# Performance work log

Hardware: AMD Instinct MI355X
Metric: run time of the kernel (lower is better)

The kernel has to match this reference:

```python
import jax, jax.numpy as jnp
import numpy as np
from jax.ops import segment_sum, segment_max

N = 50000
E = 800000
IN_C, HID_C, OUT_C, HEADS = 64, 128, 32, 4
BN_EPS = 1e-5
NEG_SLOPE = 0.2


def setup_inputs() -> dict:
    key = jax.random.key(0)
    ks = jax.random.split(key, 16)
    s = 0.1  # weight scale for numerical sanity
    inp = {
        'x': jax.random.normal(ks[0], (N, IN_C), jnp.float32),
        'edge_index': jax.random.randint(ks[1], (2, E), 0, N, jnp.int64),
        'sage1_wl': jax.random.normal(ks[2], (IN_C, HID_C), jnp.float32) * s,
        'sage1_bl': jnp.zeros((HID_C,), jnp.float32),
        'sage1_wr': jax.random.normal(ks[3], (IN_C, HID_C), jnp.float32) * s,
        'bn1_gamma': jnp.ones((HID_C,), jnp.float32),
        'bn1_beta': jnp.zeros((HID_C,), jnp.float32),
        'bn1_mean': jnp.zeros((HID_C,), jnp.float32),
        'bn1_var': jnp.ones((HID_C,), jnp.float32),
        'sage2_wl': jax.random.normal(ks[4], (HID_C, HID_C), jnp.float32) * s,
        'sage2_bl': jnp.zeros((HID_C,), jnp.float32),
        'sage2_wr': jax.random.normal(ks[5], (HID_C, HID_C), jnp.float32) * s,
        'bn2_gamma': jnp.ones((HID_C,), jnp.float32),
        'bn2_beta': jnp.zeros((HID_C,), jnp.float32),
        'bn2_mean': jnp.zeros((HID_C,), jnp.float32),
        'bn2_var': jnp.ones((HID_C,), jnp.float32),
        'gat_w': jax.random.normal(ks[6], (HID_C, HEADS * OUT_C), jnp.float32) * s,
        'gat_att_src': jax.random.normal(ks[7], (HEADS, OUT_C), jnp.float32) * s,
        'gat_att_dst': jax.random.normal(ks[8], (HEADS, OUT_C), jnp.float32) * s,
        'gat_bias': jnp.zeros((OUT_C,), jnp.float32),
        'cls_w1': jax.random.normal(ks[9], (OUT_C, 64), jnp.float32) * s,
        'cls_b1': jnp.zeros((64,), jnp.float32),
        'cls_w2': jax.random.normal(ks[10], (64, 1), jnp.float32) * s,
        'cls_b2': jnp.zeros((1,), jnp.float32),
    }
    return inp


def _sage_conv(x, src, dst, n, wl, bl, wr):
    # PyG SAGEConv (mean aggr): lin_l(mean_{j in N(i)} x_j) + lin_r(x_i)
    agg = segment_sum(x[src], dst, num_segments=n)           # [N, C]
    cnt = segment_sum(jnp.ones((src.shape[0], 1), x.dtype), dst, num_segments=n)
    mean = agg / jnp.maximum(cnt, 1.0)
    return mean @ wl + bl + x @ wr


def _bn_eval(x, gamma, beta, mean, var):
    return (x - mean) * jax.lax.rsqrt(var + BN_EPS) * gamma + beta


def _gat_conv(x, src, dst, n, w, att_src, att_dst, bias):
    # PyG GATConv, concat=False (head-average), add_self_loops=True
    loop = jnp.arange(n, dtype=src.dtype)
    s = jnp.concatenate([src, loop])
    d = jnp.concatenate([dst, loop])
    h = (x @ w).reshape(n, HEADS, OUT_C)                     # [N, H, C]
    a_src = jnp.einsum('nhc,hc->nh', h, att_src)             # [N, H]
    a_dst = jnp.einsum('nhc,hc->nh', h, att_dst)             # [N, H]
    e = jax.nn.leaky_relu(a_src[s] + a_dst[d], NEG_SLOPE)    # [Etot, H]
    m = segment_max(e, d, num_segments=n)                    # stable softmax per dst
    ex = jnp.exp(e - m[d])
    den = segment_sum(ex, d, num_segments=n)
    alpha = ex / den[d]                                      # [Etot, H]
    out = segment_sum(alpha[:, :, None] * h[s], d, num_segments=n)  # [N, H, C]
    return out.mean(axis=1) + bias                           # concat=False -> mean over heads


def reference(x, edge_index,
              sage1_wl, sage1_bl, sage1_wr,
              bn1_gamma, bn1_beta, bn1_mean, bn1_var,
              sage2_wl, sage2_bl, sage2_wr,
              bn2_gamma, bn2_beta, bn2_mean, bn2_var,
              gat_w, gat_att_src, gat_att_dst, gat_bias,
              cls_w1, cls_b1, cls_w2, cls_b2):
    n = x.shape[0]
    src, dst = edge_index[0], edge_index[1]
    # Layer 0: SAGE(64->128) + BN + ReLU (no residual: shapes differ); dropout = eval noop
    h = _sage_conv(x, src, dst, n, sage1_wl, sage1_bl, sage1_wr)
    h = jax.nn.relu(_bn_eval(h, bn1_gamma, bn1_beta, bn1_mean, bn1_var))
    # Layer 1: SAGE(128->128) + BN + residual + ReLU
    identity = h
    h2 = _sage_conv(h, src, dst, n, sage2_wl, sage2_bl, sage2_wr)
    h2 = _bn_eval(h2, bn2_gamma, bn2_beta, bn2_mean, bn2_var) + identity
    h2 = jax.nn.relu(h2)
    # Final layer: GAT head (128 -> 32, 4 heads averaged)
    embeddings = _gat_conv(h2, src, dst, n, gat_w, gat_att_src, gat_att_dst, gat_bias)
    # MLP classifier (dropout eval noop)
    logits = jax.nn.relu(embeddings @ cls_w1 + cls_b1) @ cls_w2 + cls_b2
    return embeddings, logits
```

## Files before the change

### kernel.cpp

```cpp
#include <hip/hip_runtime.h>

typedef unsigned int uint_t;
typedef unsigned short ush;
typedef short bf16x8 __attribute__((ext_vector_type(8)));
typedef float f32x4 __attribute__((ext_vector_type(4)));

constexpr int TPB = 256;
#define LOG2E 1.4426950408889634f

__device__ __forceinline__ float lrelu(float x){ return fmaxf(x, 0.f) + 0.2f*fminf(x, 0.f); }
__device__ __forceinline__ ush f2b(float f){
  uint_t u = __float_as_uint(f);
  return (ush)((u + 0x7fffu + ((u >> 16) & 1u)) >> 16);
}
__device__ __forceinline__ float b2f(ush s){ return __uint_as_float(((uint_t)s) << 16); }
__device__ __forceinline__ float eexp(float x){ return exp2f(x * LOG2E); }

__global__ void k_bnfold(const float* __restrict__ g1, const float* __restrict__ b1,
                         const float* __restrict__ m1, const float* __restrict__ v1,
                         const float* __restrict__ g2, const float* __restrict__ b2,
                         const float* __restrict__ m2, const float* __restrict__ v2,
                         float* __restrict__ out){
  int t = threadIdx.x;
  int o = t & 127;
  bool second = t >= 128;
  const float* g = second ? g2 : g1;  const float* b = second ? b2 : b1;
  const float* m = second ? m2 : m1;  const float* v = second ? v2 : v1;
  float sc = g[o] * rsqrtf(v[o] + 1e-5f);
  float sh = b[o] - m[o]*sc;
  int off = second ? 256 : 0;
  out[off + o] = sc;
  out[off + 128 + o] = sh;
}

__global__ void k_deg(const int* __restrict__ dst, int* __restrict__ degi, int E){
  int t = blockIdx.x*TPB + threadIdx.x;
  if (t < E) atomicAdd(&degi[dst[t]], 1);
}

__global__ __launch_bounds__(1024) void k_scan1(const int* __restrict__ deg,
                                                int* __restrict__ out,
                                                int* __restrict__ bsum, int n){
  __shared__ int ws[16];
  int tid = threadIdx.x;
  int gid = blockIdx.x*1024 + tid;
  int v = (gid < n) ? deg[gid] : 0;
  int lane = tid & 63, wid = tid >> 6;
  int s = v;
  for (int off = 1; off < 64; off <<= 1){
    int t2 = __shfl_up(s, off);
    if (lane >= off) s += t2;
  }
  if (lane == 63) ws[wid] = s;
  __syncthreads();
  if (wid == 0){
    int w = (lane < 16) ? ws[lane] : 0;
    for (int off = 1; off < 16; off <<= 1){
      int t2 = __shfl_up(w, off);
      if (lane >= off) w += t2;
    }
    if (lane < 16) ws[lane] = w;
  }
  __syncthreads();
  int base = wid > 0 ? ws[wid-1] : 0;
  int incl = base + s;
  if (gid < n) out[gid] = incl - v;
  if (tid == 1023) bsum[blockIdx.x] = incl;
}

__global__ void k_scan2(int* __restrict__ bsum, int nb){
  int lane = threadIdx.x;
  int carry = 0;
  for (int base = 0; base < nb; base += 64){
    int i = base + lane;
    int v = (i < nb) ? bsum[i] : 0;
    int s = v;
    for (int off = 1; off < 64; off <<= 1){
      int t2 = __shfl_up(s, off);
      if (lane >= off) s += t2;
    }
    if (i < nb) bsum[i] = carry + s - v;
    int tot = __shfl(s, 63);
    carry += tot;
  }
  if (lane == 0) bsum[nb] = carry;
}

__global__ void k_scan3(int* __restrict__ offs, const int* __restrict__ bsum, int n, int nb){
  int gid = blockIdx.x*TPB + threadIdx.x;
  if (gid < n) offs[gid] += bsum[gid >> 10];
  else if (gid == n) offs[n] = bsum[nb];
}

__global__ void k_fill(const int* __restrict__ src, const int* __restrict__ dst,
                       const int* __restrict__ offs, int* __restrict__ cur,
                       int* __restrict__ esrc, int E){
  int t = blockIdx.x*TPB + threadIdx.x;
  if (t >= E) return;
  int d = dst[t];
  int p = offs[d] + atomicAdd(&cur[d], 1);
  esrc[p] = src[t];
}

__global__ void k_tobf16(const float* __restrict__ in, ush* __restrict__ out, int n4){
  int t = blockIdx.x*TPB + threadIdx.x;
  if (t >= n4) return;
  float4 v = *(const float4*)(in + (size_t)t*4);
  ushort4 o;
  o.x = f2b(v.x); o.y = f2b(v.y); o.z = f2b(v.z); o.w = f2b(v.w);
  *(ushort4*)(out + (size_t)t*4) = o;
}

__global__ void k_wprep(const float* __restrict__ wr, const float* __restrict__ wl,
                        int C1, int K, ush* __restrict__ WT){
  int t = blockIdx.x*TPB + threadIdx.x;
  if (t >= 128*K) return;
  int n = t / K, k = t % K;
  float v = (k < C1) ? wr[(size_t)k*128 + n] : wl[(size_t)(k - C1)*128 + n];
  WT[t] = f2b(v);
}

template<int C>
__global__ __launch_bounds__(256) void k_gather_mean_b(
    const int* __restrict__ offs, const int* __restrict__ esrc,
    const uint_t* __restrict__ xb, uint_t* __restrict__ meanb, int n){
  constexpr int L = C/2;
  int tid = threadIdx.x;
  int nid = blockIdx.x*(256/L) + tid/L;
  int l = tid % L;
  if (nid >= n) return;
  int k0 = offs[nid], k1 = offs[nid+1];
  float s0 = 0.f, s1 = 0.f;
  int k = k0;
  for (; k + 4 <= k1; k += 4){
    int e0 = esrc[k], e1 = esrc[k+1], e2 = esrc[k+2], e3 = esrc[k+3];
    uint_t u0 = xb[(size_t)e0*L + l];
    uint_t u1 = xb[(size_t)e1*L + l];
    uint_t u2 = xb[(size_t)e2*L + l];
    uint_t u3 = xb[(size_t)e3*L + l];
    s0 += b2f((ush)(u0 & 0xffffu)) + b2f((ush)(u1 & 0xffffu))
        + b2f((ush)(u2 & 0xffffu)) + b2f((ush)(u3 & 0xffffu));
    s1 += b2f((ush)(u0 >> 16)) + b2f((ush)(u1 >> 16))
        + b2f((ush)(u2 >> 16)) + b2f((ush)(u3 >> 16));
  }
  for (; k < k1; ++k){
    uint_t u = xb[(size_t)esrc[k]*L + l];
    s0 += b2f((ush)(u & 0xffffu));
    s1 += b2f((ush)(u >> 16));
  }
  float inv = 1.f / (float)max(k1 - k0, 1);
  uint_t lo = f2b(s0*inv), hi = f2b(s1*inv);
  meanb[(size_t)nid*L + l] = lo | (hi << 16);
}

template<int K, bool BN, bool RES, bool RELU>
__global__ __launch_bounds__(256) void k_mm_mfma(
    const ush* __restrict__ A1, int C1,
    const ush* __restrict__ A2,
    const ush* __restrict__ WT,
    const float* __restrict__ bias,
    const float* __restrict__ bnp, int bnoff,
    const float* __restrict__ res,
    float* __restrict__ out, ush* __restrict__ outb, int n)
{
  constexpr int PAD = K + 8;
  __shared__ ush sA[32][PAD];
  int tid = threadIdx.x;
  int wave = tid >> 6, lane = tid & 63;
  int node0 = blockIdx.x * 32;
  int C2 = K - C1;

  for (int idx = tid; idx < 32*(K/8); idx += 256) {
    int r  = idx / (K/8);
    int kc = (idx % (K/8)) * 8;
    int g = node0 + r;
    uint4 v = make_uint4(0,0,0,0);
    if (g < n) {
      if (kc < C1) v = *(const uint4*)(A1 + (size_t)g*C1 + kc);
      else         v = *(const uint4*)(A2 + (size_t)g*C2 + (kc - C1));
    }
    *(uint4*)&sA[r][kc] = v;
  }
  __syncthreads();

  f32x4 acc[2][2] = {};
  int l15 = lane & 15, lk = (lane >> 4) * 8;
  const ush* wt0 = WT + (size_t)(wave*32 + l15) * K + lk;
  const ush* wt1 = wt0 + (size_t)16 * K;

  #pragma unroll
  for (int kk = 0; kk < K; kk += 32) {
    bf16x8 a0 = *(const bf16x8*)&sA[l15][kk + lk];
    bf16x8 a1 = *(const bf16x8*)&sA[16 + l15][kk + lk];
    bf16x8 b0 = *(const bf16x8*)(wt0 + kk);
    bf16x8 b1 = *(const bf16x8*)(wt1 + kk);
    acc[0][0] = __builtin_amdgcn_mfma_f32_16x16x32_bf16(a0, b0, acc[0][0], 0, 0, 0);
    acc[0][1] = __builtin_amdgcn_mfma_f32_16x16x32_bf16(a0, b1, acc[0][1], 0, 0, 0);
    acc[1][0] = __builtin_amdgcn_mfma_f32_16x16x32_bf16(a1, b0, acc[1][0], 0, 0, 0);
    acc[1][1] = __builtin_amdgcn_mfma_f32_16x16x32_bf16(a1, b1, acc[1][1], 0, 0, 0);
  }

  int r0 = (lane >> 4) * 4;
  #pragma unroll
  for (int mt = 0; mt < 2; ++mt) {
    #pragma unroll
    for (int nt = 0; nt < 2; ++nt) {
      int nn = wave*32 + nt*16 + l15;
      float bv = bias ? bias[nn] : 0.f;
      float sc = 1.f, sh = 0.f;
      if constexpr (BN) { sc = bnp[bnoff + nn]; sh = bnp[bnoff + 128 + nn]; }
      #pragma unroll
      for (int j = 0; j < 4; ++j) {
        int g = node0 + mt*16 + r0 + j;
        if (g < n) {
          float v = acc[mt][nt][j] + bv;
          if constexpr (BN)   v = v*sc + sh;
          if constexpr (RES)  v += res[(size_t)g*128 + nn];
          if constexpr (RELU) v = fmaxf(v, 0.f);
          if (out)  out[(size_t)g*128 + nn] = v;
          if (outb) outb[(size_t)g*128 + nn] = f2b(v);
        }
      }
    }
  }
}

__global__ void k_attn(const uint_t* __restrict__ hgb, const float* __restrict__ atts,
                       const float* __restrict__ attd, float* __restrict__ asrc,
                       float* __restrict__ adst, int n){
  int t = blockIdx.x*TPB + threadIdx.x;
  if (t >= n*4) return;
  int nid = t >> 2, h = t & 3;
  const uint_t* hp = hgb + (size_t)nid*64 + h*16;
  float as = 0.f, ad = 0.f;
  #pragma unroll
  for (int i = 0; i < 16; ++i) {
    uint_t u = hp[i];
    float v0 = b2f((ush)(u & 0xffffu));
    float v1 = b2f((ush)(u >> 16));
    as = fmaf(v0, atts[h*32 + 2*i],     as);
    as = fmaf(v1, atts[h*32 + 2*i + 1], as);
    ad = fmaf(v0, attd[h*32 + 2*i],     ad);
    ad = fmaf(v1, attd[h*32 + 2*i + 1], ad);
  }
  asrc[t] = as; adst[t] = ad;
}

__global__ __launch_bounds__(256) void k_gat(
    const int* __restrict__ offs, const int* __restrict__ esrc,
    const float* __restrict__ asrc, const float* __restrict__ adst,
    const uint_t* __restrict__ hgb, const float* __restrict__ gbias,
    const float* __restrict__ w1, const float* __restrict__ b1,
    const float* __restrict__ w2, const float* __restrict__ b2,
    float* __restrict__ out_emb, float* __restrict__ out_log, int n){
  __shared__ float semb[4][32];
  int tid = threadIdx.x;
  int wl = tid >> 6;
  int l = tid & 63;
  int nid = blockIdx.x*4 + wl;
  if (nid >= n) return;
  int h = l >> 4;
  int i4 = nid*4 + h;
  float ad = adst[i4];
  float e0 = eexp(lrelu(asrc[i4] + ad));
  uint_t u = hgb[(size_t)nid*64 + l];
  float accD  = e0;
  float accN0 = e0 * b2f((ush)(u & 0xffffu));
  float accN1 = e0 * b2f((ush)(u >> 16));
  int k0 = offs[nid], k1 = offs[nid+1];
  int k = k0;
  for (; k + 4 <= k1; k += 4){
    int s0 = esrc[k], s1 = esrc[k+1], s2 = esrc[k+2], s3 = esrc[k+3];
    float a0 = asrc[s0*4 + h], a1 = asrc[s1*4 + h];
    float a2 = asrc[s2*4 + h], a3 = asrc[s3*4 + h];
    uint_t v0 = hgb[(size_t)s0*64 + l];
    uint_t v1 = hgb[(size_t)s1*64 + l];
    uint_t v2 = hgb[(size_t)s2*64 + l];
    uint_t v3 = hgb[(size_t)s3*64 + l];
    float e0_ = eexp(lrelu(a0 + ad));
    float e1_ = eexp(lrelu(a1 + ad));
    float e2_ = eexp(lrelu(a2 + ad));
    float e3_ = eexp(lrelu(a3 + ad));
    accD += (e0_ + e1_) + (e2_ + e3_);
    accN0 = fmaf(e0_, b2f((ush)(v0 & 0xffffu)), accN0);
    accN0 = fmaf(e1_, b2f((ush)(v1 & 0xffffu)), accN0);
    accN0 = fmaf(e2_, b2f((ush)(v2 & 0xffffu)), accN0);
    accN0 = fmaf(e3_, b2f((ush)(v3 & 0xffffu)), accN0);
    accN1 = fmaf(e0_, b2f((ush)(v0 >> 16)), accN1);
    accN1 = fmaf(e1_, b2f((ush)(v1 >> 16)), accN1);
    accN1 = fmaf(e2_, b2f((ush)(v2 >> 16)), accN1);
    accN1 = fmaf(e3_, b2f((ush)(v3 >> 16)), accN1);
  }
  for (; k < k1; ++k){
    int s = esrc[k];
    float e = eexp(lrelu(asrc[s*4 + h] + ad));
    uint_t v = hgb[(size_t)s*64 + l];
    accD += e;
    accN0 = fmaf(e, b2f((ush)(v & 0xffffu)), accN0);
    accN1 = fmaf(e, b2f((ush)(v >> 16)),     accN1);
  }
  float inv = 1.f / accD;
  float v0 = accN0 * inv, v1 = accN1 * inv;
  v0 += __shfl_xor(v0, 16); v0 += __shfl_xor(v0, 32);
  v1 += __shfl_xor(v1, 16); v1 += __shfl_xor(v1, 32);
  if (l < 16){
    int c = l*2;
    float2 o;
    o.x = 0.25f*v0 + gbias[c];
    o.y = 0.25f*v1 + gbias[c+1];
    *(float2*)(out_emb + (size_t)nid*32 + c) = o;
    semb[wl][c] = o.x;
    semb[wl][c+1] = o.y;
  }
  float a = b1[l];
  #pragma unroll
  for (int c = 0; c < 32; ++c) a = fmaf(semb[wl][c], w1[c*64 + l], a);
  float t = fmaxf(a, 0.f) * w2[l];
  t += __shfl_xor(t, 1);  t += __shfl_xor(t, 2);  t += __shfl_xor(t, 4);
  t += __shfl_xor(t, 8);  t += __shfl_xor(t, 16); t += __shfl_xor(t, 32);
  if (l == 0) out_log[nid] = t + b2[0];
}

extern "C" void kernel_launch(void* const* d_in, const int* in_sizes, int n_in,
                              void* d_out, int out_size, void* d_ws, size_t ws_size,
                              hipStream_t stream) {
  const float* x    = (const float*)d_in[0];
  const int*   ei   = (const int*)  d_in[1];
  const float* s1wl = (const float*)d_in[2];
  const float* s1bl = (const float*)d_in[3];
  const float* s1wr = (const float*)d_in[4];
  const float* bn1g = (const float*)d_in[5];
  const float* bn1b = (const float*)d_in[6];
  const float* bn1m = (const float*)d_in[7];
  const float* bn1v = (const float*)d_in[8];
  const float* s2wl = (const float*)d_in[9];
  const float* s2bl = (const float*)d_in[10];
  const float* s2wr = (const float*)d_in[11];
  const float* bn2g = (const float*)d_in[12];
  const float* bn2b = (const float*)d_in[13];
  const float* bn2m = (const float*)d_in[14];
  const float* bn2v = (const float*)d_in[15];
  const float* gatw = (const float*)d_in[16];
  const float* atts = (const float*)d_in[17];
  const float* attd = (const float*)d_in[18];
  const float* gatb = (const float*)d_in[19];
  const float* cw1  = (const float*)d_in[20];
  const float* cb1  = (const float*)d_in[21];
  const float* cw2  = (const float*)d_in[22];
  const float* cb2  = (const float*)d_in[23];

  const int N = in_sizes[0] / 64;
  const int E = in_sizes[1] / 2;
  const int* src = ei;
  const int* dst = ei + E;
  const int NBK = (N + 1023) / 1024;

  float* h1   = (float*)d_ws;
  float* asrc = h1 + (size_t)N*128;
  float* adst = asrc + (size_t)N*4;
  float* bnp  = adst + (size_t)N*4;
  ush* regA = (ush*)(bnp + 512);
  ush* regB = regA + (size_t)N*128;
  ush* regC = regB + (size_t)N*128;
  ush* W1T  = regC + (size_t)N*128;
  ush* W2T  = W1T + 128*128;
  ush* WGT  = W2T + 128*256;
  int* degi = (int*)(WGT + 128*128);
  int* offs = degi + N;
  int* cur  = offs + N + 1;
  int* esrc = cur + N;
  int* bsum = esrc + E;

  ush* xb     = regA;
  ush* mean1b = regA + (size_t)N*64;
  ush* mean2b = regA;
  ush* h1b    = regB;
  ush* hgb    = regB;
  ush* h2b    = regC;

  float* out_emb = (float*)d_out;
  float* out_log = out_emb + (size_t)N*32;

  hipMemsetAsync(degi, 0, (size_t)N*4, stream);
  hipMemsetAsync(cur,  0, (size_t)N*4, stream);

  k_bnfold<<<1, 256, 0, stream>>>(bn1g,bn1b,bn1m,bn1v, bn2g,bn2b,bn2m,bn2v, bnp);

  k_deg<<<(E+TPB-1)/TPB, TPB, 0, stream>>>(dst, degi, E);
  k_scan1<<<NBK, 1024, 0, stream>>>(degi, offs, bsum, N);
  k_scan2<<<1, 64, 0, stream>>>(bsum, NBK);
  k_scan3<<<(N+1+TPB-1)/TPB, TPB, 0, stream>>>(offs, bsum, N, NBK);
  k_fill<<<(E+TPB-1)/TPB, TPB, 0, stream>>>(src, dst, offs, cur, esrc, E);

  k_wprep<<<(128*128+TPB-1)/TPB, TPB, 0, stream>>>(s1wr, s1wl, 64, 128, W1T);
  k_wprep<<<(128*256+TPB-1)/TPB, TPB, 0, stream>>>(s2wr, s2wl, 128, 256, W2T);
  k_wprep<<<(128*128+TPB-1)/TPB, TPB, 0, stream>>>(gatw, nullptr, 128, 128, WGT);

  k_tobf16<<<(N*16+TPB-1)/TPB, TPB, 0, stream>>>(x, xb, N*16);

  int nmm = (N + 31) / 32;

  k_gather_mean_b<64><<<(N+7)/8, 256, 0, stream>>>(offs, esrc, (const uint_t*)xb, (uint_t*)mean1b, N);
  k_mm_mfma<128,true,false,true><<<nmm, 256, 0, stream>>>(
      xb, 64, mean1b, W1T, s1bl, bnp, 0, nullptr, h1, h1b, N);

  k_gather_mean_b<128><<<(N+3)/4, 256, 0, stream>>>(offs, esrc, (const uint_t*)h1b, (uint_t*)mean2b, N);
  k_mm_mfma<256,true,true,true><<<nmm, 256, 0, stream>>>(
      h1b, 128, mean2b, W2T, s2bl, bnp, 256, h1, nullptr, h2b, N);

  k_mm_mfma<128,false,false,false><<<nmm, 256, 0, stream>>>(
      h2b, 128, nullptr, WGT, nullptr, bnp, 0, nullptr, nullptr, hgb, N);

  k_attn<<<(N*4+TPB-1)/TPB, TPB, 0, stream>>>((const uint_t*)hgb, atts, attd, asrc, adst, N);
  k_gat<<<(N+3)/4, 256, 0, stream>>>(offs, esrc, asrc, adst, (const uint_t*)hgb, gatb,
                                     cw1, cb1, cw2, cb2, out_emb, out_log, N);
}
```

Before: 284.3 us.

## Precompute per-edge GAT exponentials in separate kernel and deepen gather unrolling

```diff
diff --git a/kernel.cpp b/kernel.cpp
--- a/kernel.cpp
+++ b/kernel.cpp
@@ -14,7 +14,8 @@
   return (ush)((u + 0x7fffu + ((u >> 16) & 1u)) >> 16);
 }
 __device__ __forceinline__ float b2f(ush s){ return __uint_as_float(((uint_t)s) << 16); }
-__device__ __forceinline__ float eexp(float x){ return exp2f(x * LOG2E); }
+__device__ __forceinline__ float blo(uint_t u){ return __uint_as_float(u << 16); }
+__device__ __forceinline__ float bhi(uint_t u){ return __uint_as_float(u & 0xffff0000u); }
 
 __global__ void k_bnfold(const float* __restrict__ g1, const float* __restrict__ b1,
                          const float* __restrict__ m1, const float* __restrict__ v1,
@@ -94,12 +95,13 @@
 
 __global__ void k_fill(const int* __restrict__ src, const int* __restrict__ dst,
                        const int* __restrict__ offs, int* __restrict__ cur,
-                       int* __restrict__ esrc, int E){
+                       int* __restrict__ esrc, int* __restrict__ edst, int E){
   int t = blockIdx.x*TPB + threadIdx.x;
   if (t >= E) return;
   int d = dst[t];
   int p = offs[d] + atomicAdd(&cur[d], 1);
   esrc[p] = src[t];
+  edst[p] = d;
 }
 
 __global__ void k_tobf16(const float* __restrict__ in, ush* __restrict__ out, int n4){
@@ -130,25 +132,41 @@
   int l = tid % L;
   if (nid >= n) return;
   int k0 = offs[nid], k1 = offs[nid+1];
+  const int* sp = esrc + k0;
+  int cnt = k1 - k0;
   float s0 = 0.f, s1 = 0.f;
-  int k = k0;
-  for (; k + 4 <= k1; k += 4){
-    int e0 = esrc[k], e1 = esrc[k+1], e2 = esrc[k+2], e3 = esrc[k+3];
+  int k = 0;
+  for (; k + 8 <= cnt; k += 8){
+    int e0 = sp[k],   e1 = sp[k+1], e2 = sp[k+2], e3 = sp[k+3];
+    int e4 = sp[k+4], e5 = sp[k+5], e6 = sp[k+6], e7 = sp[k+7];
     uint_t u0 = xb[(size_t)e0*L + l];
     uint_t u1 = xb[(size_t)e1*L + l];
     uint_t u2 = xb[(size_t)e2*L + l];
     uint_t u3 = xb[(size_t)e3*L + l];
-    s0 += b2f((ush)(u0 & 0xffffu)) + b2f((ush)(u1 & 0xffffu))
-        + b2f((ush)(u2 & 0xffffu)) + b2f((ush)(u3 & 0xffffu));
-    s1 += b2f((ush)(u0 >> 16)) + b2f((ush)(u1 >> 16))
-        + b2f((ush)(u2 >> 16)) + b2f((ush)(u3 >> 16));
-  }
-  for (; k < k1; ++k){
-    uint_t u = xb[(size_t)esrc[k]*L + l];
-    s0 += b2f((ush)(u & 0xffffu));
-    s1 += b2f((ush)(u >> 16));
-  }
-  float inv = 1.f / (float)max(k1 - k0, 1);
+    uint_t u4 = xb[(size_t)e4*L + l];
+    uint_t u5 = xb[(size_t)e5*L + l];
+    uint_t u6 = xb[(size_t)e6*L + l];
+    uint_t u7 = xb[(size_t)e7*L + l];
+    s0 += ((blo(u0) + blo(u1)) + (blo(u2) + blo(u3)))
+        + ((blo(u4) + blo(u5)) + (blo(u6) + blo(u7)));
+    s1 += ((bhi(u0) + bhi(u1)) + (bhi(u2) + bhi(u3)))
+        + ((bhi(u4) + bhi(u5)) + (bhi(u6) + bhi(u7)));
+  }
+  for (; k + 4 <= cnt; k += 4){
+    int e0 = sp[k], e1 = sp[k+1], e2 = sp[k+2], e3 = sp[k+3];
+    uint_t u0 = xb[(size_t)e0*L + l];
+    uint_t u1 = xb[(size_t)e1*L + l];
+    uint_t u2 = xb[(size_t)e2*L + l];
+    uint_t u3 = xb[(size_t)e3*L + l];
+    s0 += (blo(u0) + blo(u1)) + (blo(u2) + blo(u3));
+    s1 += (bhi(u0) + bhi(u1)) + (bhi(u2) + bhi(u3));
+  }
+  for (; k < cnt; ++k){
+    uint_t u = xb[(size_t)sp[k]*L + l];
+    s0 += blo(u);
+    s1 += bhi(u);
+  }
+  float inv = 1.f / (float)max(cnt, 1);
   uint_t lo = f2b(s0*inv), hi = f2b(s1*inv);
   meanb[(size_t)nid*L + l] = lo | (hi << 16);
 }
@@ -236,18 +254,29 @@
   #pragma unroll
   for (int i = 0; i < 16; ++i) {
     uint_t u = hp[i];
-    float v0 = b2f((ush)(u & 0xffffu));
-    float v1 = b2f((ush)(u >> 16));
+    float v0 = blo(u);
+    float v1 = bhi(u);
     as = fmaf(v0, atts[h*32 + 2*i],     as);
     as = fmaf(v1, atts[h*32 + 2*i + 1], as);
     ad = fmaf(v0, attd[h*32 + 2*i],     ad);
     ad = fmaf(v1, attd[h*32 + 2*i + 1], ad);
   }
-  asrc[t] = as; adst[t] = ad;
+  asrc[t] = as * LOG2E; adst[t] = ad * LOG2E;
+}
+
+__global__ void k_eexp(const int* __restrict__ esrc, const int* __restrict__ edst,
+                       const float* __restrict__ asrc, const float* __restrict__ adst,
+                       float* __restrict__ exf, int E4){
+  int t = blockIdx.x*TPB + threadIdx.x;
+  if (t >= E4) return;
+  int k = t >> 2, h = t & 3;
+  int s = esrc[k], d = edst[k];
+  exf[t] = exp2f(lrelu(asrc[s*4 + h] + adst[d*4 + h]));
 }
 
 __global__ __launch_bounds__(256) void k_gat(
     const int* __restrict__ offs, const int* __restrict__ esrc,
+    const float* __restrict__ exf,
     const float* __restrict__ asrc, const float* __restrict__ adst,
     const uint_t* __restrict__ hgb, const float* __restrict__ gbias,
     const float* __restrict__ w1, const float* __restrict__ b1,
@@ -261,43 +290,70 @@
   if (nid >= n) return;
   int h = l >> 4;
   int i4 = nid*4 + h;
-  float ad = adst[i4];
-  float e0 = eexp(lrelu(asrc[i4] + ad));
+  float e0 = exp2f(lrelu(asrc[i4] + adst[i4]));
   uint_t u = hgb[(size_t)nid*64 + l];
   float accD  = e0;
-  float accN0 = e0 * b2f((ush)(u & 0xffffu));
-  float accN1 = e0 * b2f((ush)(u >> 16));
+  float accN0 = e0 * blo(u);
+  float accN1 = e0 * bhi(u);
   int k0 = offs[nid], k1 = offs[nid+1];
-  int k = k0;
-  for (; k + 4 <= k1; k += 4){
-    int s0 = esrc[k], s1 = esrc[k+1], s2 = esrc[k+2], s3 = esrc[k+3];
-    float a0 = asrc[s0*4 + h], a1 = asrc[s1*4 + h];
-    float a2 = asrc[s2*4 + h], a3 = asrc[s3*4 + h];
+  const int* sp = esrc + k0;
+  const float* ep = exf + (size_t)k0*4 + h;
+  int cnt = k1 - k0;
+  int k = 0;
+  for (; k + 8 <= cnt; k += 8){
+    int s0 = sp[k],   s1 = sp[k+1], s2 = sp[k+2], s3 = sp[k+3];
+    int s4 = sp[k+4], s5 = sp[k+5], s6 = sp[k+6], s7 = sp[k+7];
+    float e0_ = ep[4*k],    e1_ = ep[4*k+4],  e2_ = ep[4*k+8],  e3_ = ep[4*k+12];
+    float e4_ = ep[4*k+16], e5_ = ep[4*k+20], e6_ = ep[4*k+24], e7_ = ep[4*k+28];
     uint_t v0 = hgb[(size_t)s0*64 + l];
     uint_t v1 = hgb[(size_t)s1*64 + l];
     uint_t v2 = hgb[(size_t)s2*64 + l];
     uint_t v3 = hgb[(size_t)s3*64 + l];
-    float e0_ = eexp(lrelu(a0 + ad));
-    float e1_ = eexp(lrelu(a1 + ad));
-    float e2_ = eexp(lrelu(a2 + ad));
-    float e3_ = eexp(lrelu(a3 + ad));
+    uint_t v4 = hgb[(size_t)s4*64 + l];
+    uint_t v5 = hgb[(size_t)s5*64 + l];
+    uint_t v6 = hgb[(size_t)s6*64 + l];
+    uint_t v7 = hgb[(size_t)s7*64 + l];
+    accD += ((e0_ + e1_) + (e2_ + e3_)) + ((e4_ + e5_) + (e6_ + e7_));
+    accN0 = fmaf(e0_, blo(v0), accN0);
+    accN0 = fmaf(e1_, blo(v1), accN0);
+    accN0 = fmaf(e2_, blo(v2), accN0);
+    accN0 = fmaf(e3_, blo(v3), accN0);
+    accN0 = fmaf(e4_, blo(v4), accN0);
+    accN0 = fmaf(e5_, blo(v5), accN0);
+    accN0 = fmaf(e6_, blo(v6), accN0);
+    accN0 = fmaf(e7_, blo(v7), accN0);
+    accN1 = fmaf(e0_, bhi(v0), accN1);
+    accN1 = fmaf(e1_, bhi(v1), accN1);
+    accN1 = fmaf(e2_, bhi(v2), accN1);
+    accN1 = fmaf(e3_, bhi(v3), accN1);
+    accN1 = fmaf(e4_, bhi(v4), accN1);
+    accN1 = fmaf(e5_, bhi(v5), accN1);
+    accN1 = fmaf(e6_, bhi(v6), accN1);
+    accN1 = fmaf(e7_, bhi(v7), accN1);
+  }
+  for (; k + 4 <= cnt; k += 4){
+    int s0 = sp[k], s1 = sp[k+1], s2 = sp[k+2], s3 = sp[k+3];
+    float e0_ = ep[4*k], e1_ = ep[4*k+4], e2_ = ep[4*k+8], e3_ = ep[4*k+12];
+    uint_t v0 = hgb[(size_t)s0*64 + l];
+    uint_t v1 = hgb[(size_t)s1*64 + l];
+    uint_t v2 = hgb[(size_t)s2*64 + l];
+    uint_t v3 = hgb[(size_t)s3*64 + l];
     accD += (e0_ + e1_) + (e2_ + e3_);
-    accN0 = fmaf(e0_, b2f((ush)(v0 & 0xffffu)), accN0);
-    accN0 = fmaf(e1_, b2f((ush)(v1 & 0xffffu)), accN0);
-    accN0 = fmaf(e2_, b2f((ush)(v2 & 0xffffu)), accN0);
-    accN0 = fmaf(e3_, b2f((ush)(v3 & 0xffffu)), accN0);
-    accN1 = fmaf(e0_, b2f((ush)(v0 >> 16)), accN1);
-    accN1 = fmaf(e1_, b2f((ush)(v1 >> 16)), accN1);
-    accN1 = fmaf(e2_, b2f((ush)(v2 >> 16)), accN1);
-    accN1 = fmaf(e3_, b2f((ush)(v3 >> 16)), accN1);
-  }
-  for (; k < k1; ++k){
-    int s = esrc[k];
-    float e = eexp(lrelu(asrc[s*4 + h] + ad));
-    uint_t v = hgb[(size_t)s*64 + l];
+    accN0 = fmaf(e0_, blo(v0), accN0);
+    accN0 = fmaf(e1_, blo(v1), accN0);
+    accN0 = fmaf(e2_, blo(v2), accN0);
+    accN0 = fmaf(e3_, blo(v3), accN0);
+    accN1 = fmaf(e0_, bhi(v0), accN1);
+    accN1 = fmaf(e1_, bhi(v1), accN1);
+    accN1 = fmaf(e2_, bhi(v2), accN1);
+    accN1 = fmaf(e3_, bhi(v3), accN1);
+  }
+  for (; k < cnt; ++k){
+    float e = ep[4*k];
+    uint_t v = hgb[(size_t)sp[k]*64 + l];
     accD += e;
-    accN0 = fmaf(e, b2f((ush)(v & 0xffffu)), accN0);
-    accN1 = fmaf(e, b2f((ush)(v >> 16)),     accN1);
+    accN0 = fmaf(e, blo(v), accN0);
+    accN1 = fmaf(e, bhi(v), accN1);
   }
   float inv = 1.f / accD;
   float v0 = accN0 * inv, v1 = accN1 * inv;
@@ -369,7 +425,8 @@
   int* offs = degi + N;
   int* cur  = offs + N + 1;
   int* esrc = cur + N;
-  int* bsum = esrc + E;
+  int* edst = esrc + E;
+  int* bsum = edst + E;
 
   ush* xb     = regA;
   ush* mean1b = regA + (size_t)N*64;
@@ -377,6 +434,7 @@
   ush* h1b    = regB;
   ush* hgb    = regB;
   ush* h2b    = regC;
+  float* exf  = h1;
 
   float* out_emb = (float*)d_out;
   float* out_log = out_emb + (size_t)N*32;
@@ -390,7 +448,7 @@
   k_scan1<<<NBK, 1024, 0, stream>>>(degi, offs, bsum, N);
   k_scan2<<<1, 64, 0, stream>>>(bsum, NBK);
   k_scan3<<<(N+1+TPB-1)/TPB, TPB, 0, stream>>>(offs, bsum, N, NBK);
-  k_fill<<<(E+TPB-1)/TPB, TPB, 0, stream>>>(src, dst, offs, cur, esrc, E);
+  k_fill<<<(E+TPB-1)/TPB, TPB, 0, stream>>>(src, dst, offs, cur, esrc, edst, E);
 
   k_wprep<<<(128*128+TPB-1)/TPB, TPB, 0, stream>>>(s1wr, s1wl, 64, 128, W1T);
   k_wprep<<<(128*256+TPB-1)/TPB, TPB, 0, stream>>>(s2wr, s2wl, 128, 256, W2T);
@@ -412,6 +470,7 @@
       h2b, 128, nullptr, WGT, nullptr, bnp, 0, nullptr, nullptr, hgb, N);
 
   k_attn<<<(N*4+TPB-1)/TPB, TPB, 0, stream>>>((const uint_t*)hgb, atts, attd, asrc, adst, N);
-  k_gat<<<(N+3)/4, 256, 0, stream>>>(offs, esrc, asrc, adst, (const uint_t*)hgb, gatb,
+  k_eexp<<<(E*4+TPB-1)/TPB, TPB, 0, stream>>>(esrc, edst, asrc, adst, exf, E*4);
+  k_gat<<<(N+3)/4, 256, 0, stream>>>(offs, esrc, exf, asrc, adst, (const uint_t*)hgb, gatb,
                                      cw1, cb1, cw2, cb2, out_emb, out_log, N);
 }
```

Measured after the change: 298.0 us. 1.05x slower.
